# Kernel optimization log

Measured on AMD Instinct MI355X. Metric: run time of the kernel, lower is better.

The kernel has to match this reference:

```python
import jax, jax.numpy as jnp
import numpy as np

B, N, T, NIN, NEMB, NH = 8, 512, 64, 64, 128, 128


def _sym_normalize(A):
    # D^{-1/2} A D^{-1/2}, degree = row sum; zero-safe
    d = jnp.sum(A, axis=-1)
    dinv = jnp.where(d > 0, 1.0 / jnp.sqrt(jnp.where(d > 0, d, 1.0)), 0.0)
    return A * dinv[..., :, None] * dinv[..., None, :]


def setup_inputs() -> dict:
    key = jax.random.key(0)
    ks = jax.random.split(key, 32)
    def lin(i, fan_in, fan_out):
        s = 1.0 / np.sqrt(fan_in)
        W = jax.random.uniform(ks[2 * i], (fan_in, fan_out), jnp.float32, -s, s)
        b = jax.random.uniform(ks[2 * i + 1], (fan_out,), jnp.float32, -s, s)
        return W, b
    Wse, bse = lin(0, NIN, NEMB)
    Wpe, bpe = lin(1, NH, NEMB)
    Wii, bii = lin(2, 2 * NEMB, NH)
    Whi, bhi = lin(3, NH, NH)
    Wif, bif = lin(4, 2 * NEMB, NH)
    Whf, bhf = lin(5, NH, NH)
    Wig, big = lin(6, 2 * NEMB, NH)
    Whg, bhg = lin(7, NH, NH)
    Wio, bio = lin(8, 2 * NEMB, NH)
    Who, bho = lin(9, NH, NH)
    Wout, bout = lin(10, NH, NIN)
    X = jax.random.normal(ks[22], (B, N, T, NIN), jnp.float32)
    A = jax.random.uniform(ks[23], (B, N, N), jnp.float32)
    return dict(X=X, A=A, Wse=Wse, bse=bse, Wpe=Wpe, bpe=bpe,
                Wii=Wii, bii=bii, Whi=Whi, bhi=bhi,
                Wif=Wif, bif=bif, Whf=Whf, bhf=bhf,
                Wig=Wig, big=big, Whg=Whg, bhg=bhg,
                Wio=Wio, bio=bio, Who=Who, bho=bho,
                Wout=Wout, bout=bout)


def reference(X, A, Wse, bse, Wpe, bpe, Wii, bii, Whi, bhi, Wif, bif,
              Whf, bhf, Wig, big, Whg, bhg, Wio, bio, Who, bho, Wout, bout):
    An = _sym_normalize(A)  # [B,N,N]
    X0 = X[:, :, 0, :]                       # [B,N,NIN]
    es = X0 @ Wse + bse                      # [B,N,NEMB], constant across steps
    h0 = jnp.zeros((X.shape[0], X.shape[1], NH), X.dtype)
    c0 = jnp.zeros_like(h0)

    def step(carry, _):
        Xi, c, h = carry
        H = jnp.einsum('bnm,bmh->bnh', An, h)    # graph pooling
        eh = H @ Wpe + bpe
        x = jnp.concatenate([es, eh], axis=-1)   # [B,N,2*NEMB]
        i_t = jax.nn.sigmoid(x @ Wii + bii + h @ Whi + bhi)
        f_t = jax.nn.sigmoid(x @ Wif + bif + h @ Whf + bhf)
        g_t = jnp.tanh(x @ Wig + big + h @ Whg + bhg)
        o_t = jax.nn.sigmoid(x @ Wio + bio + h @ Who + bho)
        c_t = f_t * c + i_t * g_t
        h_t = o_t * jnp.tanh(c_t)
        Xi_new = Xi + h_t @ Wout + bout
        return (Xi_new, c_t, h_t), Xi_new

    num_steps = X.shape[2] - 1
    _, Xs = jax.lax.scan(step, (X0, c0, h0), None, length=num_steps)  # [T-1,B,N,NIN]
    X_hat = jnp.concatenate([X0[None], Xs], axis=0)                   # [T,B,N,NIN]
    return jnp.transpose(X_hat, (1, 2, 0, 3))                         # [B,N,T,NIN]
```

## Files before the change

### kernel.cpp

```cpp
#include <hip/hip_runtime.h>
#include <math.h>

#define B_ 8
#define N_ 512
#define T_ 64
#define NIN_ 64
#define NE_ 128
#define NH_ 128
#define NR_ 4096

typedef __attribute__((ext_vector_type(8))) short s8_t;
typedef __attribute__((ext_vector_type(4))) short s4_t;
typedef __attribute__((ext_vector_type(4))) float f4_t;
typedef __attribute__((ext_vector_type(4))) int i4_t;

__device__ __forceinline__ float sigm(float x) {
  x = fminf(fmaxf(x, -30.f), 30.f);
  return 1.f / (1.f + __expf(-x));
}
__device__ __forceinline__ float tanh_fast(float x) {
  x = fminf(fmaxf(x, -15.f), 15.f);
  float e = __expf(2.f * x);
  return (e - 1.f) / (e + 1.f);
}
__device__ __forceinline__ unsigned short f2b(float f) {
  union { float f; unsigned u; } v; v.f = f;
  unsigned r = (v.u + 0x7FFFu + ((v.u >> 16) & 1u)) >> 16;
  return (unsigned short)r;
}

__device__ __forceinline__ i4_t load_coherent16(const void* p) {
  i4_t r;
  asm volatile("global_load_dwordx4 %0, %1, off sc0 sc1"
               : "=v"(r) : "v"(p) : "memory");
  return r;
}
__device__ __forceinline__ void store_coherent16(void* p, i4_t v) {
  asm volatile("global_store_dwordx4 %0, %1, off sc0 sc1"
               :: "v"(p), "v"(v) : "memory");
}
__device__ __forceinline__ void wait_vm0() {
  asm volatile("s_waitcnt vmcnt(0)" ::: "memory");
}

__global__ __launch_bounds__(256) void k_setup1(
    const float* __restrict__ A,
    const float* __restrict__ bii, const float* __restrict__ bif,
    const float* __restrict__ big, const float* __restrict__ bio,
    const float* __restrict__ bhi, const float* __restrict__ bhf,
    const float* __restrict__ bhg, const float* __restrict__ bho,
    const float* __restrict__ bpe,
    const float* __restrict__ Wii, const float* __restrict__ Wif,
    const float* __restrict__ Wig, const float* __restrict__ Wio,
    const float* __restrict__ Wse, const float* __restrict__ Wout,
    float* __restrict__ dinv, float* __restrict__ bcat,
    unsigned short* __restrict__ WseP, unsigned short* __restrict__ WxeP,
    unsigned short* __restrict__ WoutP, int* __restrict__ cnt) {
  const int blk = blockIdx.x, t = threadIdx.x;
  if (blk < 1024) {
    int row = blk * 4 + (t >> 6);
    int lane = t & 63;
    const float* a = A + (size_t)row * N_;
    float s = 0.f;
    for (int j = lane; j < N_; j += 64) s += a[j];
    #pragma unroll
    for (int off = 32; off > 0; off >>= 1) s += __shfl_down(s, off);
    if (lane == 0) dinv[row] = (s > 0.f) ? rsqrtf(s) : 0.f;
  } else if (blk < 1026) {
    int col = (blk - 1024) * 256 + t;
    int g = col >> 7, j = col & 127;
    const float* bx = (g == 0) ? bii : (g == 1) ? bif : (g == 2) ? big : bio;
    const float* bh = (g == 0) ? bhi : (g == 1) ? bhf : (g == 2) ? bhg : bho;
    const float* Wx = (g == 0) ? Wii : (g == 1) ? Wif : (g == 2) ? Wig : Wio;
    float s = bx[j] + bh[j];
    for (int k = 0; k < NE_; k++) s += bpe[k] * Wx[(size_t)(128 + k) * NH_ + j];
    bcat[col] = s;
  } else if (blk < 1346) {
    int idx = (blk - 1026) * 256 + t;
    if (idx < 8192) {
      int k = idx >> 7, c = idx & 127;
      WseP[((size_t)(k >> 3) * 128 + c) * 8 + (k & 7)] = f2b(Wse[(size_t)k * 128 + c]);
    } else if (idx < 8192 + 65536) {
      int i = idx - 8192;
      int k = i >> 9, col = i & 511, g = col >> 7, j = col & 127;
      const float* Wx = (g == 0) ? Wii : (g == 1) ? Wif : (g == 2) ? Wig : Wio;
      WxeP[((size_t)(k >> 3) * 512 + col) * 8 + (k & 7)] = f2b(Wx[(size_t)k * 128 + j]);
    } else if (idx < 8192 + 65536 + 8192) {
      int i = idx - 8192 - 65536;
      int k = i >> 6, c = i & 63;
      WoutP[((size_t)(k >> 3) * 64 + c) * 8 + (k & 7)] = f2b(Wout[(size_t)k * 64 + c]);
    }
  } else {
    if (t < 128) cnt[t] = 0;
  }
}

__global__ __launch_bounds__(256) void k_setup2(
    const float* __restrict__ Wpe,
    const float* __restrict__ Whi, const float* __restrict__ Whf,
    const float* __restrict__ Whg, const float* __restrict__ Who,
    const float* __restrict__ Wii, const float* __restrict__ Wif,
    const float* __restrict__ Wig, const float* __restrict__ Wio,
    unsigned short* __restrict__ WUP2) {
  int idx = blockIdx.x * 256 + threadIdx.x;
  int k = idx >> 9, col = idx & 511, g = col >> 7, j = col & 127;
  float v;
  if (k < 128) {
    const float* Wx = (g == 0) ? Wii : (g == 1) ? Wif : (g == 2) ? Wig : Wio;
    float s = 0.f;
    for (int mm = 0; mm < 128; mm++)
      s += Wpe[(size_t)k * 128 + mm] * Wx[(size_t)(128 + mm) * 128 + j];
    v = s;
  } else {
    const float* Wh = (g == 0) ? Whi : (g == 1) ? Whf : (g == 2) ? Whg : Who;
    v = Wh[(size_t)(k - 128) * 128 + j];
  }
  WUP2[((size_t)(k >> 3) * 512 + col) * 8 + (k & 7)] = f2b(v);
}

__global__ __launch_bounds__(512, 2) void k_persist(
    const float* __restrict__ A, const float* __restrict__ dinv,
    const float* __restrict__ X,
    const unsigned short* __restrict__ WseP, const float* __restrict__ bse,
    const unsigned short* __restrict__ WxeP, const float* __restrict__ bcat,
    const unsigned short* __restrict__ WUP2,
    const unsigned short* __restrict__ WoutP, const float* __restrict__ bout,
    unsigned short* __restrict__ hP,
    int* __restrict__ cnt,
    float* __restrict__ out) {
  __shared__ __align__(16) unsigned short as[16][520];
  __shared__ __align__(16) unsigned short xh[16][264];
  __shared__ __align__(16) float zb[4][16][132];

  const int t = threadIdx.x;
  const int g = blockIdx.x;
  const int r0 = g * 16;
  const int b = g >> 5;
  const int l = t & 63, w = t >> 6, m = l & 15, kg = l >> 4;

  float* X0s = &zb[0][0][0];
  float* dvb = X0s + 1024;

  if (t < 512) dvb[t] = dinv[b * 512 + t];
  for (int i = t; i < 1024; i += 512) {
    int r = i >> 6, c = i & 63;
    float v = X[((size_t)(r0 + r) * T_) * NIN_ + c];
    X0s[i] = v;
    out[((size_t)(r0 + r) * T_) * NIN_ + c] = v;
  }
  __syncthreads();
  for (int i = t; i < 1024; i += 512) xh[i >> 6][i & 63] = f2b(X0s[i]);
  for (int i = t; i < 8192; i += 512) {
    int r = i >> 9, k = i & 511;
    as[r][k] = f2b(A[(size_t)(r0 + r) * 512 + k] * dinv[r0 + r] * dvb[k]);
  }
  __syncthreads();
  {
    f4_t e;
    float bv = bse[w * 16 + m];
    #pragma unroll
    for (int r = 0; r < 4; r++) e[r] = bv;
    #pragma unroll
    for (int kc = 0; kc < 2; kc++) {
      s8_t a = *(const s8_t*)&xh[m][kc * 32 + kg * 8];
      s8_t bf = *(const s8_t*)&WseP[((size_t)(kc * 4 + kg) * 128 + w * 16 + m) * 8];
      e = __builtin_amdgcn_mfma_f32_16x16x32_bf16(a, bf, e, 0, 0, 0);
    }
    #pragma unroll
    for (int r = 0; r < 4; r++)
      xh[kg * 4 + r][128 + w * 16 + m] = f2b(e[r]);
  }
  __syncthreads();
  f4_t esr[4];
  #pragma unroll
  for (int nt = 0; nt < 4; nt++) {
    float bv = bcat[w * 64 + nt * 16 + m];
    #pragma unroll
    for (int r = 0; r < 4; r++) esr[nt][r] = bv;
  }
  #pragma unroll
  for (int kc = 0; kc < 4; kc++) {
    s8_t a = *(const s8_t*)&xh[m][128 + kc * 32 + kg * 8];
    #pragma unroll
    for (int nt = 0; nt < 4; nt++) {
      s8_t bf = *(const s8_t*)&WxeP[((size_t)(kc * 4 + kg) * 512 + w * 64 + nt * 16 + m) * 8];
      esr[nt] = __builtin_amdgcn_mfma_f32_16x16x32_bf16(a, bf, esr[nt], 0, 0, 0);
    }
  }
  f4_t oacc = {0.f, 0.f, 0.f, 0.f};
  float bo = 0.f;
  if (w < 4) {
    bo = bout[w * 16 + m];
    #pragma unroll
    for (int r = 0; r < 4; r++) oacc[r] = X0s[(kg * 4 + r) * 64 + w * 16 + m];
  }
  float cs[4] = {0.f, 0.f, 0.f, 0.f};
  s8_t wz[8][4];
  #pragma unroll
  for (int kc = 0; kc < 8; kc++)
    #pragma unroll
    for (int nt = 0; nt < 4; nt++)
      wz[kc][nt] = *(const s8_t*)&WUP2[((size_t)(kc * 4 + kg) * 512 + w * 64 + nt * 16 + m) * 8];
  __syncthreads();
  for (int i = t; i < 16 * 264; i += 512) ((unsigned short*)xh)[i] = 0;
  __syncthreads();

  for (int tt = 1; tt < T_; tt++) {
    if (tt > 1) {
      if (t == 0) {
        const int need = 32 * (tt - 1);
        while (__hip_atomic_load(cnt + b * 16, __ATOMIC_RELAXED,
                                 __HIP_MEMORY_SCOPE_SYSTEM) < need)
          __builtin_amdgcn_s_sleep(2);
      }
      __syncthreads();
      const unsigned short* hPb =
          hP + ((size_t)((tt - 1) & 1) * 8 + b) * 65536;
      i4_t hf[16];
      #pragma unroll
      for (int kc = 0; kc < 16; kc++)
        hf[kc] = load_coherent16(
            &hPb[((size_t)(kc * 4 + kg) * 128 + w * 16 + m) * 8]);
      wait_vm0();
      f4_t ga = {0.f, 0.f, 0.f, 0.f};
      #pragma unroll
      for (int kc = 0; kc < 16; kc++) {
        s8_t a = *(const s8_t*)&as[m][kc * 32 + kg * 8];
        ga = __builtin_amdgcn_mfma_f32_16x16x32_bf16(a, *(const s8_t*)&hf[kc],
                                                     ga, 0, 0, 0);
      }
      #pragma unroll
      for (int r = 0; r < 4; r++)
        xh[kg * 4 + r][w * 16 + m] = f2b(ga[r]);
      __syncthreads();
    }
    f4_t acc[4];
    #pragma unroll
    for (int nt = 0; nt < 4; nt++) acc[nt] = esr[nt];
    #pragma unroll
    for (int kc = 0; kc < 8; kc++) {
      s8_t a = *(const s8_t*)&xh[m][kc * 32 + kg * 8];
      #pragma unroll
      for (int nt = 0; nt < 4; nt++)
        acc[nt] = __builtin_amdgcn_mfma_f32_16x16x32_bf16(a, wz[kc][nt], acc[nt], 0, 0, 0);
    }
    #pragma unroll
    for (int nt = 0; nt < 4; nt++)
      #pragma unroll
      for (int r = 0; r < 4; r++)
        zb[w >> 1][kg * 4 + r][(w & 1) * 64 + nt * 16 + m] = acc[nt][r];
    __syncthreads();
    {
      const int row = t >> 5, cg = t & 31;
      f4_t zi = *(const f4_t*)&zb[0][row][cg * 4];
      f4_t zf = *(const f4_t*)&zb[1][row][cg * 4];
      f4_t zg = *(const f4_t*)&zb[2][row][cg * 4];
      f4_t zo = *(const f4_t*)&zb[3][row][cg * 4];
      s4_t hv4;
      #pragma unroll
      for (int q = 0; q < 4; q++) {
        float it = sigm(zi[q]), ft = sigm(zf[q]);
        float gt = tanh_fast(zg[q]), ot = sigm(zo[q]);
        cs[q] = ft * cs[q] + it * gt;
        hv4[q] = (short)f2b(ot * tanh_fast(cs[q]));
      }
      *(s4_t*)&xh[row][128 + cg * 4] = hv4;
    }
    __syncthreads();
    if (tt < T_ - 1) {
      if (t < 256) {
        const int grp = t & 1, c = t >> 1;
        unsigned short tmp[8];
        #pragma unroll
        for (int q = 0; q < 8; q++) tmp[q] = xh[grp * 8 + q][128 + c];
        unsigned short* dst = hP + ((size_t)(tt & 1) * 8 + b) * 65536 +
                              ((size_t)((r0 & 511) >> 3) + grp) * 1024 +
                              (size_t)c * 8;
        store_coherent16(dst, *(i4_t*)tmp);
      }
      wait_vm0();
      __syncthreads();
      if (t == 0)
        __hip_atomic_fetch_add(cnt + b * 16, 1, __ATOMIC_RELAXED,
                               __HIP_MEMORY_SCOPE_SYSTEM);
    }
    if (w < 4) {
      f4_t o = {0.f, 0.f, 0.f, 0.f};
      #pragma unroll
      for (int kc = 0; kc < 4; kc++) {
        s8_t a = *(const s8_t*)&xh[m][128 + kc * 32 + kg * 8];
        s8_t bf = *(const s8_t*)&WoutP[((size_t)(kc * 4 + kg) * 64 + w * 16 + m) * 8];
        o = __builtin_amdgcn_mfma_f32_16x16x32_bf16(a, bf, o, 0, 0, 0);
      }
      #pragma unroll
      for (int r = 0; r < 4; r++) {
        oacc[r] += o[r] + bo;
        out[((size_t)(r0 + kg * 4 + r) * T_ + tt) * NIN_ + w * 16 + m] = oacc[r];
      }
    }
  }
}

extern "C" void kernel_launch(void* const* d_in, const int* in_sizes, int n_in,
                              void* d_out, int out_size, void* d_ws, size_t ws_size,
                              hipStream_t stream) {
  const float* X    = (const float*)d_in[0];
  const float* A    = (const float*)d_in[1];
  const float* Wse  = (const float*)d_in[2];
  const float* bse  = (const float*)d_in[3];
  const float* Wpe  = (const float*)d_in[4];
  const float* bpe  = (const float*)d_in[5];
  const float* Wii  = (const float*)d_in[6];
  const float* bii  = (const float*)d_in[7];
  const float* Whi  = (const float*)d_in[8];
  const float* bhi  = (const float*)d_in[9];
  const float* Wif  = (const float*)d_in[10];
  const float* bif_ = (const float*)d_in[11];
  const float* Whf  = (const float*)d_in[12];
  const float* bhf  = (const float*)d_in[13];
  const float* Wig  = (const float*)d_in[14];
  const float* big_ = (const float*)d_in[15];
  const float* Whg  = (const float*)d_in[16];
  const float* bhg  = (const float*)d_in[17];
  const float* Wio  = (const float*)d_in[18];
  const float* bio  = (const float*)d_in[19];
  const float* Who  = (const float*)d_in[20];
  const float* bho  = (const float*)d_in[21];
  const float* Wout = (const float*)d_in[22];
  const float* bout = (const float*)d_in[23];
  float* out = (float*)d_out;
  char* ws = (char*)d_ws;

  size_t off = 0;
  float* dinv = (float*)(ws + off);                    off += 4096 * 4;
  float* bcat = (float*)(ws + off);                    off += 512 * 4;
  unsigned short* WUP2  = (unsigned short*)(ws + off); off += 131072 * 2;
  unsigned short* WseP  = (unsigned short*)(ws + off); off += 8192 * 2;
  unsigned short* WxeP  = (unsigned short*)(ws + off); off += 65536 * 2;
  unsigned short* WoutP = (unsigned short*)(ws + off); off += 8192 * 2;
  unsigned short* hP    = (unsigned short*)(ws + off); off += (size_t)2 * 8 * 65536 * 2;
  int* cnt = (int*)(ws + off);                         off += 128 * 4;

  k_setup1<<<1347, 256, 0, stream>>>(A, bii, bif_, big_, bio, bhi, bhf, bhg,
                                     bho, bpe, Wii, Wif, Wig, Wio, Wse, Wout,
                                     dinv, bcat, WseP, WxeP, WoutP, cnt);
  k_setup2<<<512, 256, 0, stream>>>(Wpe, Whi, Whf, Whg, Who,
                                    Wii, Wif, Wig, Wio, WUP2);

  void* args[] = {(void*)&A, (void*)&dinv, (void*)&X,
                  (void*)&WseP, (void*)&bse, (void*)&WxeP, (void*)&bcat,
                  (void*)&WUP2, (void*)&WoutP, (void*)&bout,
                  (void*)&hP, (void*)&cnt, (void*)&out};
  if (hipLaunchCooperativeKernel((const void*)k_persist, dim3(256), dim3(512),
                                 args, 0, stream) != hipSuccess) {
    k_persist<<<256, 512, 0, stream>>>(A, dinv, X, WseP, bse, WxeP, bcat,
                                       WUP2, WoutP, bout, hP, cnt, out);
  }
}
```

Measured before the change: 626.5 us.

## Compute LSTM gates in registers and store h directly, cutting barriers and LDS round-trips

The gate-to-wave mapping now gives each wave one 16-column slice of all four gates, so the LSTM cell update runs directly on the MFMA accumulators. This removes the zb LDS staging buffer and one barrier per step. Each lane writes its bf16 h fragment straight to global memory with an 8-byte coherent store. All threads now poll the counter instead of thread 0 followed by a barrier, the h loads are waited on in two halves so MFMAs can start early, and the block-to-batch mapping is interleaved. In exchange there are more, smaller global stores and more polling traffic on the counter.

```diff
diff --git a/kernel.cpp b/kernel.cpp
--- a/kernel.cpp
+++ b/kernel.cpp
@@ -13,6 +13,7 @@
 typedef __attribute__((ext_vector_type(4))) short s4_t;
 typedef __attribute__((ext_vector_type(4))) float f4_t;
 typedef __attribute__((ext_vector_type(4))) int i4_t;
+typedef __attribute__((ext_vector_type(2))) int i2_t;
 
 __device__ __forceinline__ float sigm(float x) {
   x = fminf(fmaxf(x, -30.f), 30.f);
@@ -35,8 +36,8 @@
                : "=v"(r) : "v"(p) : "memory");
   return r;
 }
-__device__ __forceinline__ void store_coherent16(void* p, i4_t v) {
-  asm volatile("global_store_dwordx4 %0, %1, off sc0 sc1"
+__device__ __forceinline__ void store_coherent8(void* p, i2_t v) {
+  asm volatile("global_store_dwordx2 %0, %1, off sc0 sc1"
                :: "v"(p), "v"(v) : "memory");
 }
 __device__ __forceinline__ void wait_vm0() {
@@ -130,23 +131,24 @@
     float* __restrict__ out) {
   __shared__ __align__(16) unsigned short as[16][520];
   __shared__ __align__(16) unsigned short xh[16][264];
-  __shared__ __align__(16) float zb[4][16][132];
+  __shared__ __align__(16) float ps[1536];
 
   const int t = threadIdx.x;
-  const int g = blockIdx.x;
-  const int r0 = g * 16;
-  const int b = g >> 5;
+  const int b = blockIdx.x & 7;
+  const int rt = blockIdx.x >> 3;
+  const int r0 = b * N_ + rt * 16;
   const int l = t & 63, w = t >> 6, m = l & 15, kg = l >> 4;
-
-  float* X0s = &zb[0][0][0];
-  float* dvb = X0s + 1024;
+  const int c = w * 16 + m;
+
+  float* X0s = ps;
+  float* dvb = ps + 1024;
 
   if (t < 512) dvb[t] = dinv[b * 512 + t];
   for (int i = t; i < 1024; i += 512) {
-    int r = i >> 6, c = i & 63;
-    float v = X[((size_t)(r0 + r) * T_) * NIN_ + c];
+    int r = i >> 6, cc = i & 63;
+    float v = X[((size_t)(r0 + r) * T_) * NIN_ + cc];
     X0s[i] = v;
-    out[((size_t)(r0 + r) * T_) * NIN_ + c] = v;
+    out[((size_t)(r0 + r) * T_) * NIN_ + cc] = v;
   }
   __syncthreads();
   for (int i = t; i < 1024; i += 512) xh[i >> 6][i & 63] = f2b(X0s[i]);
@@ -157,34 +159,34 @@
   __syncthreads();
   {
     f4_t e;
-    float bv = bse[w * 16 + m];
+    float bv = bse[c];
     #pragma unroll
     for (int r = 0; r < 4; r++) e[r] = bv;
     #pragma unroll
     for (int kc = 0; kc < 2; kc++) {
       s8_t a = *(const s8_t*)&xh[m][kc * 32 + kg * 8];
-      s8_t bf = *(const s8_t*)&WseP[((size_t)(kc * 4 + kg) * 128 + w * 16 + m) * 8];
+      s8_t bf = *(const s8_t*)&WseP[((size_t)(kc * 4 + kg) * 128 + c) * 8];
       e = __builtin_amdgcn_mfma_f32_16x16x32_bf16(a, bf, e, 0, 0, 0);
     }
     #pragma unroll
     for (int r = 0; r < 4; r++)
-      xh[kg * 4 + r][128 + w * 16 + m] = f2b(e[r]);
+      xh[kg * 4 + r][128 + c] = f2b(e[r]);
   }
   __syncthreads();
   f4_t esr[4];
   #pragma unroll
-  for (int nt = 0; nt < 4; nt++) {
-    float bv = bcat[w * 64 + nt * 16 + m];
-    #pragma unroll
-    for (int r = 0; r < 4; r++) esr[nt][r] = bv;
+  for (int g = 0; g < 4; g++) {
+    float bv = bcat[g * 128 + c];
+    #pragma unroll
+    for (int r = 0; r < 4; r++) esr[g][r] = bv;
   }
   #pragma unroll
   for (int kc = 0; kc < 4; kc++) {
     s8_t a = *(const s8_t*)&xh[m][128 + kc * 32 + kg * 8];
     #pragma unroll
-    for (int nt = 0; nt < 4; nt++) {
-      s8_t bf = *(const s8_t*)&WxeP[((size_t)(kc * 4 + kg) * 512 + w * 64 + nt * 16 + m) * 8];
-      esr[nt] = __builtin_amdgcn_mfma_f32_16x16x32_bf16(a, bf, esr[nt], 0, 0, 0);
+    for (int g = 0; g < 4; g++) {
+      s8_t bf = *(const s8_t*)&WxeP[((size_t)(kc * 4 + kg) * 512 + g * 128 + c) * 8];
+      esr[g] = __builtin_amdgcn_mfma_f32_16x16x32_bf16(a, bf, esr[g], 0, 0, 0);
     }
   }
   f4_t oacc = {0.f, 0.f, 0.f, 0.f};
@@ -199,91 +201,83 @@
   #pragma unroll
   for (int kc = 0; kc < 8; kc++)
     #pragma unroll
-    for (int nt = 0; nt < 4; nt++)
-      wz[kc][nt] = *(const s8_t*)&WUP2[((size_t)(kc * 4 + kg) * 512 + w * 64 + nt * 16 + m) * 8];
+    for (int g = 0; g < 4; g++)
+      wz[kc][g] = *(const s8_t*)&WUP2[((size_t)(kc * 4 + kg) * 512 + g * 128 + c) * 8];
   __syncthreads();
   for (int i = t; i < 16 * 264; i += 512) ((unsigned short*)xh)[i] = 0;
   __syncthreads();
 
   for (int tt = 1; tt < T_; tt++) {
     if (tt > 1) {
-      if (t == 0) {
-        const int need = 32 * (tt - 1);
-        while (__hip_atomic_load(cnt + b * 16, __ATOMIC_RELAXED,
-                                 __HIP_MEMORY_SCOPE_SYSTEM) < need)
-          __builtin_amdgcn_s_sleep(2);
-      }
-      __syncthreads();
+      const int need = 32 * (tt - 1);
+      while (__hip_atomic_load(cnt + b * 16, __ATOMIC_RELAXED,
+                               __HIP_MEMORY_SCOPE_SYSTEM) < need)
+        __builtin_amdgcn_s_sleep(1);
       const unsigned short* hPb =
           hP + ((size_t)((tt - 1) & 1) * 8 + b) * 65536;
       i4_t hf[16];
       #pragma unroll
       for (int kc = 0; kc < 16; kc++)
-        hf[kc] = load_coherent16(
-            &hPb[((size_t)(kc * 4 + kg) * 128 + w * 16 + m) * 8]);
-      wait_vm0();
+        hf[kc] = load_coherent16(&hPb[((size_t)(kc * 4 + kg) * 128 + c) * 8]);
       f4_t ga = {0.f, 0.f, 0.f, 0.f};
-      #pragma unroll
-      for (int kc = 0; kc < 16; kc++) {
+      asm volatile("s_waitcnt vmcnt(8)"
+                   : "+v"(hf[0]), "+v"(hf[1]), "+v"(hf[2]), "+v"(hf[3]),
+                     "+v"(hf[4]), "+v"(hf[5]), "+v"(hf[6]), "+v"(hf[7])
+                   :: "memory");
+      #pragma unroll
+      for (int kc = 0; kc < 8; kc++) {
         s8_t a = *(const s8_t*)&as[m][kc * 32 + kg * 8];
         ga = __builtin_amdgcn_mfma_f32_16x16x32_bf16(a, *(const s8_t*)&hf[kc],
                                                      ga, 0, 0, 0);
       }
+      asm volatile("s_waitcnt vmcnt(0)"
+                   : "+v"(hf[8]), "+v"(hf[9]), "+v"(hf[10]), "+v"(hf[11]),
+                     "+v"(hf[12]), "+v"(hf[13]), "+v"(hf[14]), "+v"(hf[15])
+                   :: "memory");
+      #pragma unroll
+      for (int kc = 8; kc < 16; kc++) {
+        s8_t a = *(const s8_t*)&as[m][kc * 32 + kg * 8];
+        ga = __builtin_amdgcn_mfma_f32_16x16x32_bf16(a, *(const s8_t*)&hf[kc],
+                                                     ga, 0, 0, 0);
+      }
       #pragma unroll
       for (int r = 0; r < 4; r++)
-        xh[kg * 4 + r][w * 16 + m] = f2b(ga[r]);
+        xh[kg * 4 + r][c] = f2b(ga[r]);
       __syncthreads();
     }
     f4_t acc[4];
     #pragma unroll
-    for (int nt = 0; nt < 4; nt++) acc[nt] = esr[nt];
+    for (int g = 0; g < 4; g++) acc[g] = esr[g];
     #pragma unroll
     for (int kc = 0; kc < 8; kc++) {
       s8_t a = *(const s8_t*)&xh[m][kc * 32 + kg * 8];
       #pragma unroll
-      for (int nt = 0; nt < 4; nt++)
-        acc[nt] = __builtin_amdgcn_mfma_f32_16x16x32_bf16(a, wz[kc][nt], acc[nt], 0, 0, 0);
-    }
-    #pragma unroll
-    for (int nt = 0; nt < 4; nt++)
-      #pragma unroll
-      for (int r = 0; r < 4; r++)
-        zb[w >> 1][kg * 4 + r][(w & 1) * 64 + nt * 16 + m] = acc[nt][r];
+      for (int g = 0; g < 4; g++)
+        acc[g] = __builtin_amdgcn_mfma_f32_16x16x32_bf16(a, wz[kc][g], acc[g], 0, 0, 0);
+    }
+    union { unsigned short u[4]; i2_t v; } hb;
+    #pragma unroll
+    for (int r = 0; r < 4; r++) {
+      float it = sigm(acc[0][r]), ft = sigm(acc[1][r]);
+      float gt = tanh_fast(acc[2][r]), ot = sigm(acc[3][r]);
+      cs[r] = ft * cs[r] + it * gt;
+      hb.u[r] = f2b(ot * tanh_fast(cs[r]));
+    }
+    if (tt < T_ - 1) {
+      unsigned short* dst = hP + ((size_t)(tt & 1) * 8 + b) * 65536 +
+                            (size_t)(rt * 2 + (kg >> 1)) * 1024 +
+                            (size_t)c * 8 + (kg & 1) * 4;
+      store_coherent8(dst, hb.v);
+    }
     __syncthreads();
-    {
-      const int row = t >> 5, cg = t & 31;
-      f4_t zi = *(const f4_t*)&zb[0][row][cg * 4];
-      f4_t zf = *(const f4_t*)&zb[1][row][cg * 4];
-      f4_t zg = *(const f4_t*)&zb[2][row][cg * 4];
-      f4_t zo = *(const f4_t*)&zb[3][row][cg * 4];
-      s4_t hv4;
-      #pragma unroll
-      for (int q = 0; q < 4; q++) {
-        float it = sigm(zi[q]), ft = sigm(zf[q]);
-        float gt = tanh_fast(zg[q]), ot = sigm(zo[q]);
-        cs[q] = ft * cs[q] + it * gt;
-        hv4[q] = (short)f2b(ot * tanh_fast(cs[q]));
-      }
-      *(s4_t*)&xh[row][128 + cg * 4] = hv4;
-    }
+    #pragma unroll
+    for (int r = 0; r < 4; r++)
+      xh[kg * 4 + r][128 + c] = hb.u[r];
+    if (tt < T_ - 1) wait_vm0();
     __syncthreads();
-    if (tt < T_ - 1) {
-      if (t < 256) {
-        const int grp = t & 1, c = t >> 1;
-        unsigned short tmp[8];
-        #pragma unroll
-        for (int q = 0; q < 8; q++) tmp[q] = xh[grp * 8 + q][128 + c];
-        unsigned short* dst = hP + ((size_t)(tt & 1) * 8 + b) * 65536 +
-                              ((size_t)((r0 & 511) >> 3) + grp) * 1024 +
-                              (size_t)c * 8;
-        store_coherent16(dst, *(i4_t*)tmp);
-      }
-      wait_vm0();
-      __syncthreads();
-      if (t == 0)
-        __hip_atomic_fetch_add(cnt + b * 16, 1, __ATOMIC_RELAXED,
-                               __HIP_MEMORY_SCOPE_SYSTEM);
-    }
+    if (tt < T_ - 1 && t == 0)
+      __hip_atomic_fetch_add(cnt + b * 16, 1, __ATOMIC_RELAXED,
+                             __HIP_MEMORY_SCOPE_SYSTEM);
     if (w < 4) {
       f4_t o = {0.f, 0.f, 0.f, 0.f};
       #pragma unroll
```

Measured after the change: 597.5 us. 4.6% less time.
